# Optimization experiments

Measured on AMD Instinct MI355X. Metric: run time of the kernel, lower is better.

## Reference

```python
import jax, jax.numpy as jnp
import numpy as np

B, S, D = 4, 2048, 1024


def setup_inputs() -> dict:
    key = jax.random.key(0)
    k1, k2, k3, k4 = jax.random.split(key, 4)
    x = jax.random.normal(k1, (B, S, D), dtype=jnp.float32)
    # 'random_normal' keras initializer uses stddev=0.05
    w_keys = jax.random.normal(k2, (D, D), dtype=jnp.float32) * 0.05
    w_queries = jax.random.normal(k3, (D, D), dtype=jnp.float32) * 0.05
    w_values = jax.random.normal(k4, (D, D), dtype=jnp.float32) * 0.05
    return {"x": x, "w_keys": w_keys, "w_queries": w_queries, "w_values": w_values}


def reference(x, w_keys, w_queries, w_values):
    # fact = sqrt(input feature dim)
    fact = jnp.sqrt(jnp.asarray(x.shape[-1], x.dtype))
    vk = x @ w_keys      # [B,S,D]
    vq = x @ w_queries   # [B,S,D]
    vv = x @ w_values    # [B,S,D]
    # NOTE: module computes K @ Q^T (keys as rows), softmax over last axis
    kq = jnp.einsum('bsd,btd->bst', vk, vq) / fact   # [B,S,S]
    sn = jax.nn.softmax(kq, axis=-1)
    # pm + transpose_b cancel: out = sn @ vv
    out = jnp.einsum('bst,btd->bsd', sn, vv)         # [B,S,D]
    return out
```

## Files before the change

### kernel.cpp

```cpp
#include <hip/hip_runtime.h>


typedef __attribute__((ext_vector_type(8))) short bf16x8;
typedef __attribute__((ext_vector_type(4))) float f32x4;

__device__ __forceinline__ unsigned short f2bf(float f) {
    unsigned int u = __float_as_uint(f);
    u += 0x7fff + ((u >> 16) & 1);
    return (unsigned short)(u >> 16);
}

__device__ __forceinline__ void gld_lds16(const unsigned short* g, unsigned short* l) {
    __builtin_amdgcn_global_load_lds(
        (const __attribute__((address_space(1))) void*)g,
        (__attribute__((address_space(3))) void*)l, 16, 0, 0);
}

template<int N> __device__ __forceinline__ void vmcnt_wait() {
    if constexpr (N == 0) asm volatile("s_waitcnt vmcnt(0)" ::: "memory");
    else if constexpr (N == 8) asm volatile("s_waitcnt vmcnt(8)" ::: "memory");
}
__device__ __forceinline__ void bar() {
    asm volatile("" ::: "memory");
    __builtin_amdgcn_s_barrier();
    asm volatile("" ::: "memory");
}

template<int KT, bool RS>
__device__ __forceinline__ void gemm4(
    const unsigned short* __restrict__ A, const unsigned short* __restrict__ B,
    int lda, int ldb, int bm, int bn,
    unsigned short* As, unsigned short* Bs,
    f32x4 (&acc)[4][4], f32x4 (&os)[4])
{
    const int tid  = threadIdx.x;
    const int lane = tid & 63;
    const int wave = tid >> 6;
    const int wr = wave >> 1, wc = wave & 1;
    const int lr = lane & 15, kg = lane >> 4;

    const bf16x8 ONES = { (short)0x3F80, (short)0x3F80, (short)0x3F80, (short)0x3F80,
                          (short)0x3F80, (short)0x3F80, (short)0x3F80, (short)0x3F80 };

    const int srow = tid >> 2;
    const int ssrc = ((tid & 3) ^ ((tid >> 3) & 3)) * 8;
    const unsigned short* pa0 = A + (size_t)(bm + srow) * lda + ssrc;
    const unsigned short* pa1 = A + (size_t)(bm + 64 + srow) * lda + ssrc;
    const unsigned short* pb0 = B + (size_t)(bn + srow) * ldb + ssrc;
    const unsigned short* pb1 = B + (size_t)(bn + 64 + srow) * ldb + ssrc;

    const int phys = (kg ^ ((lr >> 1) & 3)) * 8;
    const int aoff = (wr * 64 + lr) * 32 + phys;
    const int boff = (wc * 64 + lr) * 32 + phys;

    auto stage = [&](int buf, int kt) {
        unsigned short* da = As + buf * 8192 + wave * 512;
        unsigned short* db = Bs + buf * 8192 + wave * 512;
        #pragma unroll
        for (int kh = 0; kh < 2; kh++) {
            const int go = kt * 64 + kh * 32;
            gld_lds16(pa0 + go, da + kh * 4096);
            gld_lds16(pa1 + go, da + kh * 4096 + 2048);
            gld_lds16(pb0 + go, db + kh * 4096);
            gld_lds16(pb1 + go, db + kh * 4096 + 2048);
        }
    };

    stage(0, 0);
    stage(1, 1);
    vmcnt_wait<8>();
    bar();

    for (int kt = 0; kt < KT; ++kt) {
        const int c = kt & 1;
        const unsigned short* Ab = As + c * 8192 + aoff;
        const unsigned short* Bb = Bs + c * 8192 + boff;

        #pragma unroll
        for (int kh = 0; kh < 2; kh++) {
            bf16x8 af[4], bf[4];
            #pragma unroll
            for (int mf = 0; mf < 4; mf++)
                af[mf] = *reinterpret_cast<const bf16x8*>(Ab + kh * 4096 + mf * 512);
            #pragma unroll
            for (int nf = 0; nf < 4; nf++)
                bf[nf] = *reinterpret_cast<const bf16x8*>(Bb + kh * 4096 + nf * 512);
            __builtin_amdgcn_s_setprio(1);
            #pragma unroll
            for (int mf = 0; mf < 4; mf++)
                #pragma unroll
                for (int nf = 0; nf < 4; nf++)
                    acc[mf][nf] = __builtin_amdgcn_mfma_f32_16x16x32_bf16(af[mf], bf[nf], acc[mf][nf], 0, 0, 0);
            if constexpr (RS) {
                #pragma unroll
                for (int mf = 0; mf < 4; mf++)
                    os[mf] = __builtin_amdgcn_mfma_f32_16x16x32_bf16(af[mf], ONES, os[mf], 0, 0, 0);
            }
            __builtin_amdgcn_s_setprio(0);
        }

        if (kt == KT - 1) break;
        bar();
        if (kt + 2 < KT) {
            stage(c, kt + 2);
            vmcnt_wait<8>();
        } else {
            vmcnt_wait<0>();
        }
        bar();
    }
}

__global__ __launch_bounds__(256) void stage1(
    const float* __restrict__ x,  unsigned short* __restrict__ xb,
    const float* __restrict__ wv, unsigned short* __restrict__ wvT,
    const float* __restrict__ wq, const float* __restrict__ wk,
    unsigned short* __restrict__ Gt)
{
    __shared__ unsigned short SM[4608];
    const int bid = blockIdx.x;
    const int tid = threadIdx.x;

    if (bid >= 256 && bid < 4352) {
        const size_t idx = (size_t)(bid - 256) * 256 + tid;
        const float4* xi = reinterpret_cast<const float4*>(x) + idx * 2;
        float4 v0 = xi[0], v1 = xi[1];
        ushort4 a = { f2bf(v0.x), f2bf(v0.y), f2bf(v0.z), f2bf(v0.w) };
        ushort4 b = { f2bf(v1.x), f2bf(v1.y), f2bf(v1.z), f2bf(v1.w) };
        ushort4* xo = reinterpret_cast<ushort4*>(xb) + idx * 2;
        xo[0] = a; xo[1] = b;
        return;
    }
    if (bid >= 4352) {
        auto T = reinterpret_cast<unsigned short (*)[72]>(SM);
        const int tb = bid - 4352;
        const int k0 = (tb >> 4) * 64, n0 = (tb & 15) * 64;
        const int r = tid >> 4, c4 = (tid & 15) * 4;
        #pragma unroll
        for (int i = 0; i < 4; i++) {
            int kr = r + i * 16;
            float4 v = *reinterpret_cast<const float4*>(&wv[(size_t)(k0 + kr) * 1024 + n0 + c4]);
            T[c4 + 0][kr] = f2bf(v.x);
            T[c4 + 1][kr] = f2bf(v.y);
            T[c4 + 2][kr] = f2bf(v.z);
            T[c4 + 3][kr] = f2bf(v.w);
        }
        __syncthreads();
        #pragma unroll
        for (int i = 0; i < 4; i++) {
            int n = r + i * 16;
            ushort4 v = *reinterpret_cast<const ushort4*>(&T[n][c4]);
            *reinterpret_cast<ushort4*>(&wvT[(size_t)(n0 + n) * 1024 + k0 + c4]) = v;
        }
        return;
    }

    unsigned short* As = SM;
    unsigned short* Bs = SM + 2048;
    const int gb = bid;
    const int bm = (gb >> 4) * 64, bn = (gb & 15) * 64;

    const int lane = tid & 63;
    const int wave = tid >> 6;
    const int wr = wave >> 1, wc = wave & 1;
    const int lr = lane & 15, kg = lane >> 4;

    const int srow = tid >> 2;
    const int su   = tid & 3;
    const int sphys = (su ^ ((srow >> 1) & 3)) * 8;
    const int rphys = (kg ^ ((lr >> 1) & 3)) * 8;
    const int aoff = (wr * 32 + lr) * 32 + rphys;
    const int boff = (wc * 32 + lr) * 32 + rphys;

    const float* pa = &wq[(size_t)(bm + srow) * 1024 + su * 8];
    const float* pb = &wk[(size_t)(bn + srow) * 1024 + su * 8];

    f32x4 acc[2][2] = {};

    float4 a0 = *reinterpret_cast<const float4*>(pa);
    float4 a1 = *reinterpret_cast<const float4*>(pa + 4);
    float4 b0 = *reinterpret_cast<const float4*>(pb);
    float4 b1 = *reinterpret_cast<const float4*>(pb + 4);

    for (int k0 = 0; k0 < 1024; k0 += 32) {
        ushort4 u0 = { f2bf(a0.x), f2bf(a0.y), f2bf(a0.z), f2bf(a0.w) };
        ushort4 u1 = { f2bf(a1.x), f2bf(a1.y), f2bf(a1.z), f2bf(a1.w) };
        *reinterpret_cast<ushort4*>(&As[srow * 32 + sphys])     = u0;
        *reinterpret_cast<ushort4*>(&As[srow * 32 + sphys + 4]) = u1;
        ushort4 t0 = { f2bf(b0.x), f2bf(b0.y), f2bf(b0.z), f2bf(b0.w) };
        ushort4 t1 = { f2bf(b1.x), f2bf(b1.y), f2bf(b1.z), f2bf(b1.w) };
        *reinterpret_cast<ushort4*>(&Bs[srow * 32 + sphys])     = t0;
        *reinterpret_cast<ushort4*>(&Bs[srow * 32 + sphys + 4]) = t1;

        if (k0 + 32 < 1024) {
            const float* npa = pa + k0 + 32;
            const float* npb = pb + k0 + 32;
            a0 = *reinterpret_cast<const float4*>(npa);
            a1 = *reinterpret_cast<const float4*>(npa + 4);
            b0 = *reinterpret_cast<const float4*>(npb);
            b1 = *reinterpret_cast<const float4*>(npb + 4);
        }
        __syncthreads();

        bf16x8 af[2], bf[2];
        #pragma unroll
        for (int mf = 0; mf < 2; mf++)
            af[mf] = *reinterpret_cast<const bf16x8*>(&As[aoff + mf * 512]);
        #pragma unroll
        for (int nf = 0; nf < 2; nf++)
            bf[nf] = *reinterpret_cast<const bf16x8*>(&Bs[boff + nf * 512]);
        #pragma unroll
        for (int mf = 0; mf < 2; mf++)
            #pragma unroll
            for (int nf = 0; nf < 2; nf++)
                acc[mf][nf] = __builtin_amdgcn_mfma_f32_16x16x32_bf16(af[mf], bf[nf], acc[mf][nf], 0, 0, 0);
        __syncthreads();
    }
    #pragma unroll
    for (int mf = 0; mf < 2; mf++)
        #pragma unroll
        for (int nf = 0; nf < 2; nf++)
            #pragma unroll
            for (int r = 0; r < 4; r++)
                Gt[(size_t)(bm + wr * 32 + mf * 16 + kg * 4 + r) * 1024
                   + bn + wc * 32 + nf * 16 + lr] = f2bf(acc[mf][nf][r]);
}

__global__ __launch_bounds__(256, 2) void proj_gemm(
    const unsigned short* __restrict__ xb, const unsigned short* __restrict__ Gt,
    const unsigned short* __restrict__ wvT,
    unsigned short* __restrict__ y, unsigned short* __restrict__ vvT)
{
    __shared__ unsigned short As[2 * 128 * 64], Bs[2 * 128 * 64];
    const int bid = blockIdx.x;
    const int wg  = (bid & 7) * 128 + (bid >> 3);
    const int z   = wg >> 9;
    const int rem = wg & 511;
    const int bm  = (rem >> 3) * 128;
    const int bn  = (rem & 7) * 128;
    const unsigned short* Bw = z ? wvT : Gt;

    f32x4 acc[4][4] = {};
    f32x4 os[4] = {};
    gemm4<16, false>(xb, Bw, 1024, 1024, bm, bn, As, Bs, acc, os);

    const int tid = threadIdx.x, lane = tid & 63, wave = tid >> 6;
    const int wr = wave >> 1, wc = wave & 1, lr = lane & 15, kg = lane >> 4;
    if (z == 0) {
        #pragma unroll
        for (int mf = 0; mf < 4; mf++)
            #pragma unroll
            for (int nf = 0; nf < 4; nf++)
                #pragma unroll
                for (int r = 0; r < 4; r++)
                    y[(size_t)(bm + wr * 64 + mf * 16 + kg * 4 + r) * 1024
                      + bn + wc * 64 + nf * 16 + lr] = f2bf(acc[mf][nf][r]);
    } else {
        const int batch = bm >> 11;
        unsigned short* o = vvT + (size_t)batch * 1024 * 2048;
        #pragma unroll
        for (int mf = 0; mf < 4; mf++)
            #pragma unroll
            for (int nf = 0; nf < 4; nf++) {
                ushort4 v = { f2bf(acc[mf][nf][0]), f2bf(acc[mf][nf][1]),
                              f2bf(acc[mf][nf][2]), f2bf(acc[mf][nf][3]) };
                *reinterpret_cast<ushort4*>(
                    &o[(size_t)(bn + wc * 64 + nf * 16 + lr) * 2048
                       + (bm & 2047) + wr * 64 + mf * 16 + kg * 4]) = v;
            }
    }
}

__global__ __launch_bounds__(256, 2) void scores_gemm(
    const unsigned short* __restrict__ y, const unsigned short* __restrict__ xb,
    unsigned short* __restrict__ P)
{
    __shared__ unsigned short As[2 * 128 * 64], Bs[2 * 128 * 64];
    const int bid = blockIdx.x;
    const int wg  = (bid & 7) * 128 + (bid >> 3);
    const int z   = wg >> 8;
    const int rem = wg & 255;
    const int bm  = (rem >> 4) * 128;
    const int bn  = (rem & 15) * 128;
    const unsigned short* A = y  + (size_t)z * 2048 * 1024;
    const unsigned short* B = xb + (size_t)z * 2048 * 1024;
    unsigned short* out = P + (size_t)z * 2048 * 2048;

    f32x4 acc[4][4] = {};
    f32x4 os[4] = {};
    gemm4<16, false>(A, B, 1024, 1024, bm, bn, As, Bs, acc, os);

    const int tid = threadIdx.x, lane = tid & 63, wave = tid >> 6;
    const int wr = wave >> 1, wc = wave & 1, lr = lane & 15, kg = lane >> 4;
    #pragma unroll
    for (int mf = 0; mf < 4; mf++)
        #pragma unroll
        for (int nf = 0; nf < 4; nf++)
            #pragma unroll
            for (int r = 0; r < 4; r++)
                out[(size_t)(bm + wr * 64 + mf * 16 + kg * 4 + r) * 2048
                    + bn + wc * 64 + nf * 16 + lr]
                    = f2bf(__expf(acc[mf][nf][r] * 0.03125f));
}

__global__ __launch_bounds__(256, 2) void pv_gemm(
    const unsigned short* __restrict__ P, const unsigned short* __restrict__ vvT,
    float* __restrict__ out)
{
    __shared__ unsigned short As[2 * 128 * 64], Bs[2 * 128 * 64];
    const int bid = blockIdx.x;
    const int wg  = (bid & 7) * 64 + (bid >> 3);
    const int z   = wg >> 7;
    const int rem = wg & 127;
    const int bm  = (rem >> 3) * 128;
    const int bn  = (rem & 7) * 128;
    const unsigned short* A = P   + (size_t)z * 2048 * 2048;
    const unsigned short* B = vvT + (size_t)z * 1024 * 2048;
    float* o = out + (size_t)z * 2048 * 1024;

    f32x4 acc[4][4] = {};
    f32x4 os[4] = {};
    gemm4<32, true>(A, B, 2048, 2048, bm, bn, As, Bs, acc, os);

    const int tid = threadIdx.x, lane = tid & 63, wave = tid >> 6;
    const int wr = wave >> 1, wc = wave & 1, lr = lane & 15, kg = lane >> 4;

    #pragma unroll
    for (int mf = 0; mf < 4; mf++)
        #pragma unroll
        for (int r = 0; r < 4; r++) {
            const float inv = 1.0f / os[mf][r];
            #pragma unroll
            for (int nf = 0; nf < 4; nf++)
                o[(size_t)(bm + wr * 64 + mf * 16 + kg * 4 + r) * 1024
                  + bn + wc * 64 + nf * 16 + lr] = acc[mf][nf][r] * inv;
        }
}

extern "C" void kernel_launch(void* const* d_in, const int* in_sizes, int n_in,
                              void* d_out, int out_size, void* d_ws, size_t ws_size,
                              hipStream_t stream) {
    const float* x  = (const float*)d_in[0];
    const float* wk = (const float*)d_in[1];
    const float* wq = (const float*)d_in[2];
    const float* wv = (const float*)d_in[3];
    float* out = (float*)d_out;

    char* ws = (char*)d_ws;
    const size_t MB = 1024 * 1024;
    unsigned short* xb  = (unsigned short*)(ws);
    unsigned short* y   = (unsigned short*)(ws + 16 * MB);
    unsigned short* Gt  = (unsigned short*)(ws + 32 * MB);
    unsigned short* wvT = (unsigned short*)(ws + 34 * MB);
    unsigned short* vvT = (unsigned short*)(ws + 36 * MB);
    unsigned short* P   = (unsigned short*)(ws + 52 * MB);

    stage1     <<<dim3(4608), 256, 0, stream>>>(x, xb, wv, wvT, wq, wk, Gt);
    proj_gemm  <<<dim3(1024), 256, 0, stream>>>(xb, Gt, wvT, y, vvT);
    scores_gemm<<<dim3(1024), 256, 0, stream>>>(y, xb, P);
    pv_gemm    <<<dim3(512),  256, 0, stream>>>(P, vvT, out);
}
```

Measured before the change: 156.0 us.

## Widen GEMM block tiles to 128x256 with a K-step of 32

Replaces the 128x128 block tile with a 128x256 tile for the projection, scores and PV GEMMs. Each wave now computes 64x128 outputs per step, and the per-stage K depth is halved to 32 so shared memory stays the same size. The aim is more MFMA work per LDS and A-operand load, and less redundant global traffic. In exchange, accumulator registers double, the two-blocks-per-CU launch bound is dropped, and the grids halve, so occupancy and CU fill may drop, especially in pv_gemm with 256 blocks.

```diff
diff --git a/kernel.cpp b/kernel.cpp
--- a/kernel.cpp
+++ b/kernel.cpp
@@ -18,7 +18,7 @@
 
 template<int N> __device__ __forceinline__ void vmcnt_wait() {
     if constexpr (N == 0) asm volatile("s_waitcnt vmcnt(0)" ::: "memory");
-    else if constexpr (N == 8) asm volatile("s_waitcnt vmcnt(8)" ::: "memory");
+    else if constexpr (N == 6) asm volatile("s_waitcnt vmcnt(6)" ::: "memory");
 }
 __device__ __forceinline__ void bar() {
     asm volatile("" ::: "memory");
@@ -27,11 +27,11 @@
 }
 
 template<int KT, bool RS>
-__device__ __forceinline__ void gemm4(
+__device__ __forceinline__ void gemm_wide(
     const unsigned short* __restrict__ A, const unsigned short* __restrict__ B,
     int lda, int ldb, int bm, int bn,
     unsigned short* As, unsigned short* Bs,
-    f32x4 (&acc)[4][4], f32x4 (&os)[4])
+    f32x4 (&acc)[4][8], f32x4 (&os)[4])
 {
     const int tid  = threadIdx.x;
     const int lane = tid & 63;
@@ -48,62 +48,68 @@
     const unsigned short* pa1 = A + (size_t)(bm + 64 + srow) * lda + ssrc;
     const unsigned short* pb0 = B + (size_t)(bn + srow) * ldb + ssrc;
     const unsigned short* pb1 = B + (size_t)(bn + 64 + srow) * ldb + ssrc;
+    const unsigned short* pb2 = B + (size_t)(bn + 128 + srow) * ldb + ssrc;
+    const unsigned short* pb3 = B + (size_t)(bn + 192 + srow) * ldb + ssrc;
 
     const int phys = (kg ^ ((lr >> 1) & 3)) * 8;
     const int aoff = (wr * 64 + lr) * 32 + phys;
-    const int boff = (wc * 64 + lr) * 32 + phys;
+    const int boff = (wc * 128 + lr) * 32 + phys;
 
     auto stage = [&](int buf, int kt) {
-        unsigned short* da = As + buf * 8192 + wave * 512;
+        unsigned short* da = As + buf * 4096 + wave * 512;
         unsigned short* db = Bs + buf * 8192 + wave * 512;
-        #pragma unroll
-        for (int kh = 0; kh < 2; kh++) {
-            const int go = kt * 64 + kh * 32;
-            gld_lds16(pa0 + go, da + kh * 4096);
-            gld_lds16(pa1 + go, da + kh * 4096 + 2048);
-            gld_lds16(pb0 + go, db + kh * 4096);
-            gld_lds16(pb1 + go, db + kh * 4096 + 2048);
-        }
+        const int go = kt * 32;
+        gld_lds16(pa0 + go, da);
+        gld_lds16(pa1 + go, da + 2048);
+        gld_lds16(pb0 + go, db);
+        gld_lds16(pb1 + go, db + 2048);
+        gld_lds16(pb2 + go, db + 4096);
+        gld_lds16(pb3 + go, db + 6144);
     };
 
     stage(0, 0);
     stage(1, 1);
-    vmcnt_wait<8>();
+    vmcnt_wait<6>();
     bar();
 
     for (int kt = 0; kt < KT; ++kt) {
         const int c = kt & 1;
-        const unsigned short* Ab = As + c * 8192 + aoff;
+        const unsigned short* Ab = As + c * 4096 + aoff;
         const unsigned short* Bb = Bs + c * 8192 + boff;
 
-        #pragma unroll
-        for (int kh = 0; kh < 2; kh++) {
-            bf16x8 af[4], bf[4];
+        bf16x8 af[4], bh[4];
+        #pragma unroll
+        for (int mf = 0; mf < 4; mf++)
+            af[mf] = *reinterpret_cast<const bf16x8*>(Ab + mf * 512);
+        #pragma unroll
+        for (int j = 0; j < 4; j++)
+            bh[j] = *reinterpret_cast<const bf16x8*>(Bb + j * 512);
+        __builtin_amdgcn_s_setprio(1);
+        #pragma unroll
+        for (int mf = 0; mf < 4; mf++)
+            #pragma unroll
+            for (int j = 0; j < 4; j++)
+                acc[mf][j] = __builtin_amdgcn_mfma_f32_16x16x32_bf16(af[mf], bh[j], acc[mf][j], 0, 0, 0);
+        #pragma unroll
+        for (int j = 0; j < 4; j++)
+            bh[j] = *reinterpret_cast<const bf16x8*>(Bb + (4 + j) * 512);
+        #pragma unroll
+        for (int mf = 0; mf < 4; mf++)
+            #pragma unroll
+            for (int j = 0; j < 4; j++)
+                acc[mf][4 + j] = __builtin_amdgcn_mfma_f32_16x16x32_bf16(af[mf], bh[j], acc[mf][4 + j], 0, 0, 0);
+        if constexpr (RS) {
             #pragma unroll
             for (int mf = 0; mf < 4; mf++)
-                af[mf] = *reinterpret_cast<const bf16x8*>(Ab + kh * 4096 + mf * 512);
-            #pragma unroll
-            for (int nf = 0; nf < 4; nf++)
-                bf[nf] = *reinterpret_cast<const bf16x8*>(Bb + kh * 4096 + nf * 512);
-            __builtin_amdgcn_s_setprio(1);
-            #pragma unroll
-            for (int mf = 0; mf < 4; mf++)
-                #pragma unroll
-                for (int nf = 0; nf < 4; nf++)
-                    acc[mf][nf] = __builtin_amdgcn_mfma_f32_16x16x32_bf16(af[mf], bf[nf], acc[mf][nf], 0, 0, 0);
-            if constexpr (RS) {
-                #pragma unroll
-                for (int mf = 0; mf < 4; mf++)
-                    os[mf] = __builtin_amdgcn_mfma_f32_16x16x32_bf16(af[mf], ONES, os[mf], 0, 0, 0);
-            }
-            __builtin_amdgcn_s_setprio(0);
-        }
+                os[mf] = __builtin_amdgcn_mfma_f32_16x16x32_bf16(af[mf], ONES, os[mf], 0, 0, 0);
+        }
+        __builtin_amdgcn_s_setprio(0);
 
         if (kt == KT - 1) break;
         bar();
         if (kt + 2 < KT) {
             stage(c, kt + 2);
-            vmcnt_wait<8>();
+            vmcnt_wait<6>();
         } else {
             vmcnt_wait<0>();
         }
@@ -226,23 +232,23 @@
                    + bn + wc * 32 + nf * 16 + lr] = f2bf(acc[mf][nf][r]);
 }
 
-__global__ __launch_bounds__(256, 2) void proj_gemm(
+__global__ __launch_bounds__(256) void proj_gemm(
     const unsigned short* __restrict__ xb, const unsigned short* __restrict__ Gt,
     const unsigned short* __restrict__ wvT,
     unsigned short* __restrict__ y, unsigned short* __restrict__ vvT)
 {
-    __shared__ unsigned short As[2 * 128 * 64], Bs[2 * 128 * 64];
+    __shared__ unsigned short As[2 * 128 * 32], Bs[2 * 256 * 32];
     const int bid = blockIdx.x;
-    const int wg  = (bid & 7) * 128 + (bid >> 3);
-    const int z   = wg >> 9;
-    const int rem = wg & 511;
-    const int bm  = (rem >> 3) * 128;
-    const int bn  = (rem & 7) * 128;
+    const int wg  = (bid & 7) * 64 + (bid >> 3);
+    const int z   = wg >> 8;
+    const int rem = wg & 255;
+    const int bm  = (rem >> 2) * 128;
+    const int bn  = (rem & 3) * 256;
     const unsigned short* Bw = z ? wvT : Gt;
 
-    f32x4 acc[4][4] = {};
+    f32x4 acc[4][8] = {};
     f32x4 os[4] = {};
-    gemm4<16, false>(xb, Bw, 1024, 1024, bm, bn, As, Bs, acc, os);
+    gemm_wide<32, false>(xb, Bw, 1024, 1024, bm, bn, As, Bs, acc, os);
 
     const int tid = threadIdx.x, lane = tid & 63, wave = tid >> 6;
     const int wr = wave >> 1, wc = wave & 1, lr = lane & 15, kg = lane >> 4;
@@ -250,77 +256,77 @@
         #pragma unroll
         for (int mf = 0; mf < 4; mf++)
             #pragma unroll
-            for (int nf = 0; nf < 4; nf++)
+            for (int nf = 0; nf < 8; nf++)
                 #pragma unroll
                 for (int r = 0; r < 4; r++)
                     y[(size_t)(bm + wr * 64 + mf * 16 + kg * 4 + r) * 1024
-                      + bn + wc * 64 + nf * 16 + lr] = f2bf(acc[mf][nf][r]);
+                      + bn + wc * 128 + nf * 16 + lr] = f2bf(acc[mf][nf][r]);
     } else {
         const int batch = bm >> 11;
         unsigned short* o = vvT + (size_t)batch * 1024 * 2048;
         #pragma unroll
         for (int mf = 0; mf < 4; mf++)
             #pragma unroll
-            for (int nf = 0; nf < 4; nf++) {
+            for (int nf = 0; nf < 8; nf++) {
                 ushort4 v = { f2bf(acc[mf][nf][0]), f2bf(acc[mf][nf][1]),
                               f2bf(acc[mf][nf][2]), f2bf(acc[mf][nf][3]) };
                 *reinterpret_cast<ushort4*>(
-                    &o[(size_t)(bn + wc * 64 + nf * 16 + lr) * 2048
+                    &o[(size_t)(bn + wc * 128 + nf * 16 + lr) * 2048
                        + (bm & 2047) + wr * 64 + mf * 16 + kg * 4]) = v;
             }
     }
 }
 
-__global__ __launch_bounds__(256, 2) void scores_gemm(
+__global__ __launch_bounds__(256) void scores_gemm(
     const unsigned short* __restrict__ y, const unsigned short* __restrict__ xb,
     unsigned short* __restrict__ P)
 {
-    __shared__ unsigned short As[2 * 128 * 64], Bs[2 * 128 * 64];
-    const int bid = blockIdx.x;
-    const int wg  = (bid & 7) * 128 + (bid >> 3);
-    const int z   = wg >> 8;
-    const int rem = wg & 255;
-    const int bm  = (rem >> 4) * 128;
-    const int bn  = (rem & 15) * 128;
-    const unsigned short* A = y  + (size_t)z * 2048 * 1024;
-    const unsigned short* B = xb + (size_t)z * 2048 * 1024;
-    unsigned short* out = P + (size_t)z * 2048 * 2048;
-
-    f32x4 acc[4][4] = {};
-    f32x4 os[4] = {};
-    gemm4<16, false>(A, B, 1024, 1024, bm, bn, As, Bs, acc, os);
-
-    const int tid = threadIdx.x, lane = tid & 63, wave = tid >> 6;
-    const int wr = wave >> 1, wc = wave & 1, lr = lane & 15, kg = lane >> 4;
-    #pragma unroll
-    for (int mf = 0; mf < 4; mf++)
-        #pragma unroll
-        for (int nf = 0; nf < 4; nf++)
-            #pragma unroll
-            for (int r = 0; r < 4; r++)
-                out[(size_t)(bm + wr * 64 + mf * 16 + kg * 4 + r) * 2048
-                    + bn + wc * 64 + nf * 16 + lr]
-                    = f2bf(__expf(acc[mf][nf][r] * 0.03125f));
-}
-
-__global__ __launch_bounds__(256, 2) void pv_gemm(
-    const unsigned short* __restrict__ P, const unsigned short* __restrict__ vvT,
-    float* __restrict__ out)
-{
-    __shared__ unsigned short As[2 * 128 * 64], Bs[2 * 128 * 64];
+    __shared__ unsigned short As[2 * 128 * 32], Bs[2 * 256 * 32];
     const int bid = blockIdx.x;
     const int wg  = (bid & 7) * 64 + (bid >> 3);
     const int z   = wg >> 7;
     const int rem = wg & 127;
     const int bm  = (rem >> 3) * 128;
-    const int bn  = (rem & 7) * 128;
+    const int bn  = (rem & 7) * 256;
+    const unsigned short* A = y  + (size_t)z * 2048 * 1024;
+    const unsigned short* B = xb + (size_t)z * 2048 * 1024;
+    unsigned short* out = P + (size_t)z * 2048 * 2048;
+
+    f32x4 acc[4][8] = {};
+    f32x4 os[4] = {};
+    gemm_wide<32, false>(A, B, 1024, 1024, bm, bn, As, Bs, acc, os);
+
+    const int tid = threadIdx.x, lane = tid & 63, wave = tid >> 6;
+    const int wr = wave >> 1, wc = wave & 1, lr = lane & 15, kg = lane >> 4;
+    #pragma unroll
+    for (int mf = 0; mf < 4; mf++)
+        #pragma unroll
+        for (int nf = 0; nf < 8; nf++)
+            #pragma unroll
+            for (int r = 0; r < 4; r++)
+                out[(size_t)(bm + wr * 64 + mf * 16 + kg * 4 + r) * 2048
+                    + bn + wc * 128 + nf * 16 + lr]
+                    = f2bf(__expf(acc[mf][nf][r] * 0.03125f));
+}
+
+__global__ __launch_bounds__(256) void pv_gemm(
+    const unsigned short* __restrict__ P, const unsigned short* __restrict__ vvT,
+    float* __restrict__ out)
+{
+    __shared__ unsigned short As[2 * 128 * 32], Bs[2 * 256 * 32];
+    const int bid = blockIdx.x;
+    const int wg  = (bid & 7) * 32 + (bid >> 3);
+    const int z   = wg >> 6;
+    const int rem = wg & 63;
+    const int bm  = (rem >> 2) * 128;
+    const int bn  = (rem & 3) * 256;
     const unsigned short* A = P   + (size_t)z * 2048 * 2048;
     const unsigned short* B = vvT + (size_t)z * 1024 * 2048;
     float* o = out + (size_t)z * 2048 * 1024;
 
-    f32x4 acc[4][4] = {};
+    f32x4 acc[4][8] = {};
     f32x4 os[4] = {};
-    gemm4<32, true>(A, B, 2048, 2048, bm, bn, As, Bs, acc, os);
+    gemm_wide<64, true>(A, B, 2048, 2048, bm, bn, As, Bs, acc, os);
 
     const int tid = threadIdx.x, lane = tid & 63, wave = tid >> 6;
     const int wr = wave >> 1, wc = wave & 1, lr = lane & 15, kg = lane >> 4;
@@ -331,9 +337,9 @@
         for (int r = 0; r < 4; r++) {
             const float inv = 1.0f / os[mf][r];
             #pragma unroll
-            for (int nf = 0; nf < 4; nf++)
+            for (int nf = 0; nf < 8; nf++)
                 o[(size_t)(bm + wr * 64 + mf * 16 + kg * 4 + r) * 1024
-                  + bn + wc * 64 + nf * 16 + lr] = acc[mf][nf][r] * inv;
+                  + bn + wc * 128 + nf * 16 + lr] = acc[mf][nf][r] * inv;
         }
 }
 
@@ -356,7 +362,7 @@
     unsigned short* P   = (unsigned short*)(ws + 52 * MB);
 
     stage1     <<<dim3(4608), 256, 0, stream>>>(x, xb, wv, wvT, wq, wk, Gt);
-    proj_gemm  <<<dim3(1024), 256, 0, stream>>>(xb, Gt, wvT, y, vvT);
-    scores_gemm<<<dim3(1024), 256, 0, stream>>>(y, xb, P);
-    pv_gemm    <<<dim3(512),  256, 0, stream>>>(P, vvT, out);
-}
+    proj_gemm  <<<dim3(512),  256, 0, stream>>>(xb, Gt, wvT, y, vvT);
+    scores_gemm<<<dim3(512),  256, 0, stream>>>(y, xb, P);
+    pv_gemm    <<<dim3(256),  256, 0, stream>>>(P, vvT, out);
+}
```

Result: slower. 235.3 us (+50.9%).
